# Optimization experiments

Measured on AMD Instinct MI355X. Metric: run time of the kernel, lower is better.

Reference implementation:

```python
import jax, jax.numpy as jnp
import numpy as np

IN_CH = 512
PROP_CH = 512
T_FEAT = 16384
T_FRAME = 32768
GROUPS = 32
EPS = 1e-5


def conv1x1(x, w, b):
    # x: (B, Cin, T), w: (Cout, Cin), b: (Cout,)
    return jnp.einsum('bct,oc->bot', x, w) + b[None, :, None]


def group_norm(x, gamma, beta):
    bsz, c, t = x.shape
    xg = x.reshape(bsz, GROUPS, c // GROUPS, t)
    mean = jnp.mean(xg, axis=(2, 3), keepdims=True)
    var = jnp.var(xg, axis=(2, 3), keepdims=True)
    xn = ((xg - mean) * jax.lax.rsqrt(var + EPS)).reshape(bsz, c, t)
    return xn * gamma[None, :, None] + beta[None, :, None]


def block(x, w, b, g, bt):
    # _Unit1D(k=1, act=None) -> GroupNorm(32) -> ReLU
    return jax.nn.relu(group_norm(conv1x1(x, w, b), g, bt))


def setup_inputs() -> dict:
    key = jax.random.key(0)
    ks = jax.random.split(key, 5)
    return dict(
        feature=jax.random.normal(ks[0], (1, IN_CH, T_FEAT), jnp.float32),
        frame_level_feature=jax.random.normal(ks[1], (1, IN_CH, T_FRAME), jnp.float32),
        cur_w=jax.random.normal(ks[2], (PROP_CH, IN_CH), jnp.float32) * 0.02,
        cur_b=jnp.zeros((PROP_CH,), jnp.float32),
        gn1_g=jnp.ones((PROP_CH,), jnp.float32),
        gn1_b=jnp.zeros((PROP_CH,), jnp.float32),
        lr_w=jax.random.normal(ks[3], (PROP_CH * 2, IN_CH), jnp.float32) * 0.02,
        lr_b=jnp.zeros((PROP_CH * 2,), jnp.float32),
        gn2_g=jnp.ones((PROP_CH * 2,), jnp.float32),
        gn2_b=jnp.zeros((PROP_CH * 2,), jnp.float32),
        prop_w=jax.random.normal(ks[4], (IN_CH, PROP_CH * 4), jnp.float32) * 0.02,
        prop_b=jnp.zeros((IN_CH,), jnp.float32),
        gn3_g=jnp.ones((IN_CH,), jnp.float32),
        gn3_b=jnp.zeros((IN_CH,), jnp.float32),
    )


def reference(feature, frame_level_feature, cur_w, cur_b, gn1_g, gn1_b,
              lr_w, lr_b, gn2_g, gn2_b, prop_w, prop_b, gn3_g, gn3_b):
    fm_short = block(feature, cur_w, cur_b, gn1_g, gn1_b)   # (1, P, t)
    feat = block(feature, lr_w, lr_b, gn2_g, gn2_b)         # (1, 2P, t)
    t = feat.shape[2]

    # ---- inverse-CDF sampling, vectorized equivalent of the original loop ----
    max_values = jnp.max(frame_level_feature, axis=1)        # (1, T)
    max_values = max_values / jnp.sum(max_values)
    cdf = jnp.cumsum(max_values, axis=1)[0]                  # (T,)
    c = (cdf * t).astype(jnp.int32)                          # trunc toward 0, like .int()
    # In the original, cur_idx advances only while no bin matches and is
    # never advanced after a successful match, so EVERY iteration i picks
    # the FIRST index whose bin equals the smallest value >= 0 present in c.
    big = jnp.iinfo(jnp.int32).max
    cur = jnp.min(jnp.where(c >= 0, c, big))
    idx = jnp.argmax(c == cur)                               # first occurrence
    col = jax.lax.dynamic_index_in_dim(frame_level_feature, idx, axis=2)  # (1, C, 1)
    sampled = jnp.broadcast_to(col, (col.shape[0], col.shape[1], t))      # (1, C, t)

    mixed = jnp.concatenate([sampled, feat, fm_short], axis=1)  # (1, 4P, t)
    mixed = block(mixed, prop_w, prop_b, gn3_g, gn3_b)          # (1, Cin, t)
    return mixed, feat
```

## Files before the change

### kernel.cpp

```cpp
#include <hip/hip_runtime.h>
#include <hip/hip_bf16.h>
#include <cstdint>
#include <cstddef>

#define TN   16384
#define TFR  32768
#define K1   512
#define M12  1536
#define M3   512

#define NSLOT 64

typedef __attribute__((ext_vector_type(8))) short short8;
typedef __attribute__((ext_vector_type(4))) float f32x4;

__device__ __forceinline__ unsigned short f2bf(float f) {
  __hip_bfloat16 h = __float2bfloat16(f);
  unsigned short u; __builtin_memcpy(&u, &h, 2); return u;
}
__device__ __forceinline__ float bf2f(unsigned short u) {
  __hip_bfloat16 h; __builtin_memcpy(&h, &u, 2); return __bfloat162float(h);
}

__global__ void prep_w(const float* __restrict__ cur_w, const float* __restrict__ cur_b,
                       const float* __restrict__ lr_w, const float* __restrict__ lr_b,
                       const float* __restrict__ prop_w,
                       unsigned short* __restrict__ w12, unsigned short* __restrict__ w3,
                       float* __restrict__ b12) {
  int i = blockIdx.x * blockDim.x + threadIdx.x;
  {
    int r = i >> 9, k = i & 511;
    float v = (r < 1024) ? lr_w[i] : cur_w[(r - 1024) * 512 + k];
    w12[i] = f2bf(v);
  }
  {
    int o = i / 1536, c = i - o * 1536;
    w3[i] = f2bf(prop_w[o * 2048 + 512 + c]);
  }
  if (i < M12) b12[i] = (i < 1024) ? lr_b[i] : cur_b[i - 1024];
}

__global__ void maxred(const float* __restrict__ fr, float* __restrict__ pm) {
  int b = blockIdx.x;
  int cchunk = b >> 7;
  int t = (b & 127) * 256 + threadIdx.x;
  int cs = cchunk * 64;
  float mx = -3.4e38f;
#pragma unroll 8
  for (int c = cs; c < cs + 64; ++c) mx = fmaxf(mx, fr[(size_t)c * TFR + t]);
  pm[(size_t)cchunk * TFR + t] = mx;
}

__global__ __launch_bounds__(1024) void scan_pick(const float* __restrict__ pm,
                                                  int* __restrict__ idxp) {
  __shared__ float sA[1024], sB[1024];
  __shared__ int si[1024];
  int tid = threadIdx.x;
  int base = tid * 32;
  float mv[32];
  float lsum = 0.f;
#pragma unroll
  for (int j = 0; j < 32; ++j) {
    int t = base + j;
    float mx = pm[t];
#pragma unroll
    for (int p = 1; p < 8; ++p) mx = fmaxf(mx, pm[(size_t)p * TFR + t]);
    mv[j] = mx; lsum += mx;
  }
  sA[tid] = lsum; __syncthreads();
  float* a = sA; float* b = sB;
  for (int d = 1; d < 1024; d <<= 1) {
    float v = a[tid];
    if (tid >= d) v += a[tid - d];
    b[tid] = v; __syncthreads();
    float* tmp = a; a = b; b = tmp;
  }
  float total = a[1023];
  float prev = (tid > 0) ? a[tid - 1] : 0.f;
  float inv = 1.0f / total;
  int cloc[32];
  int minc = 0x7fffffff;
  float run = prev;
#pragma unroll
  for (int j = 0; j < 32; ++j) {
    run += mv[j];
    int cj = (int)(run * inv * 16384.0f);
    cloc[j] = cj;
    if (cj >= 0 && cj < minc) minc = cj;
  }
  si[tid] = minc; __syncthreads();
  for (int d = 512; d >= 1; d >>= 1) { if (tid < d) si[tid] = min(si[tid], si[tid + d]); __syncthreads(); }
  int cur = si[0]; __syncthreads();
  int cand = 0x7fffffff;
#pragma unroll
  for (int j = 0; j < 32; ++j)
    if (cloc[j] == cur && cand == 0x7fffffff) cand = base + j;
  si[tid] = cand; __syncthreads();
  for (int d = 512; d >= 1; d >>= 1) { if (tid < d) si[tid] = min(si[tid], si[tid + d]); __syncthreads(); }
  if (tid == 0) idxp[0] = si[0];
}

__global__ void sample_const(const float* __restrict__ prop_w, const float* __restrict__ prop_b,
                             const float* __restrict__ frame, const int* __restrict__ idxp,
                             float* __restrict__ constb) {
  int o = blockIdx.x * blockDim.x + threadIdx.x;
  if (o >= 512) return;
  int idx = idxp[0];
  float acc = prop_b[o];
  for (int c = 0; c < 512; ++c)
    acc += prop_w[o * 2048 + c] * frame[(size_t)c * TFR + idx];
  constb[o] = acc;
}

__global__ __launch_bounds__(256) void transpose_feat(const float* __restrict__ X,
                                                      unsigned short* __restrict__ XT) {
  __shared__ float tile[64][65];
  int t0 = blockIdx.x * 64, c0 = blockIdx.y * 64;
  int tx = threadIdx.x & 63, ty = threadIdx.x >> 6;
#pragma unroll
  for (int r = 0; r < 16; ++r) {
    int c = c0 + ty * 16 + r;
    tile[ty * 16 + r][tx] = X[(size_t)c * TN + t0 + tx];
  }
  __syncthreads();
#pragma unroll
  for (int r = 0; r < 16; ++r) {
    int t = t0 + ty * 16 + r;
    XT[(size_t)t * K1 + c0 + tx] = f2bf(tile[tx][ty * 16 + r]);
  }
}

__global__ __launch_bounds__(256) void gemm_bf16(
    const unsigned short* __restrict__ XT,
    const unsigned short* __restrict__ Wb,
    const float* __restrict__ bias,
    unsigned short* __restrict__ Y,
    float* __restrict__ gsum, float* __restrict__ gss,
    int K, int M, int mode)
{
  __shared__ __attribute__((aligned(16))) unsigned short As[128 * 64];
  __shared__ __attribute__((aligned(16))) unsigned short Bs[128 * 64];
  const int tid = threadIdx.x;
  const int lane = tid & 63;
  const int w = tid >> 6;
  const int t0 = blockIdx.x * 128;
  const int c0 = blockIdx.y * 128;

  f32x4 acc[4][4] = {};
  const int lrow = lane & 15;
  const int lk = (lane >> 4) * 8;
  const int tb = (w >> 1) * 64, cb = (w & 1) * 64;

  const int Lbase = w * 4096 + lane * 16;
  const int srow0 = Lbase >> 7;
  const int scolb = (Lbase & 127) ^ ((srow0 & 7) << 4);

  for (int ks = 0; ks < K; ks += 64) {
    __syncthreads();
#pragma unroll
    for (int it = 0; it < 4; ++it) {
      int row = srow0 + it * 8;
      const char* ga = (const char*)(XT + (size_t)(t0 + row) * K + ks) + scolb;
      const char* gb = (const char*)(Wb + (size_t)(c0 + row) * K + ks) + scolb;
      char* la = (char*)As + w * 4096 + it * 1024;
      char* lb = (char*)Bs + w * 4096 + it * 1024;
      __builtin_amdgcn_global_load_lds(
          (const __attribute__((address_space(1))) unsigned int*)ga,
          (__attribute__((address_space(3))) unsigned int*)la, 16, 0, 0);
      __builtin_amdgcn_global_load_lds(
          (const __attribute__((address_space(1))) unsigned int*)gb,
          (__attribute__((address_space(3))) unsigned int*)lb, 16, 0, 0);
    }
    __syncthreads();
#pragma unroll
    for (int kk = 0; kk < 64; kk += 32) {
      short8 a[4], b[4];
#pragma unroll
      for (int i = 0; i < 4; ++i) {
        int r = tb + i * 16 + lrow;
        int cbyte = ((kk + lk) * 2) ^ ((r & 7) << 4);
        a[i] = *(const short8*)((const char*)As + r * 128 + cbyte);
      }
#pragma unroll
      for (int j = 0; j < 4; ++j) {
        int r = cb + j * 16 + lrow;
        int cbyte = ((kk + lk) * 2) ^ ((r & 7) << 4);
        b[j] = *(const short8*)((const char*)Bs + r * 128 + cbyte);
      }
#pragma unroll
      for (int i = 0; i < 4; ++i)
#pragma unroll
        for (int j = 0; j < 4; ++j)
          acc[i][j] = __builtin_amdgcn_mfma_f32_16x16x32_bf16(a[i], b[j], acc[i][j], 0, 0, 0);
    }
  }

  const int lq = (lane >> 4) * 4;
  const int slot = blockIdx.x & (NSLOT - 1);
#pragma unroll
  for (int j = 0; j < 4; ++j) {
    int c = c0 + cb + j * 16 + lrow;
    float bv = bias[c];
    float s = 0.f, ss = 0.f;
#pragma unroll
    for (int i = 0; i < 4; ++i) {
#pragma unroll
      for (int q = 0; q < 4; ++q) {
        float v = acc[i][j][q] + bv;
        s += v; ss += v * v;
        int t = t0 + tb + i * 16 + lq + q;
        Y[(size_t)t * M + c] = f2bf(v);
      }
    }
#pragma unroll
    for (int off = 32; off >= 1; off >>= 1) { s += __shfl_xor(s, off); ss += __shfl_xor(ss, off); }
    if (lane == 0) {
      int g = (mode == 0) ? ((c < 1024) ? (c >> 5) : (32 + ((c - 1024) >> 4))) : (c >> 4);
      atomicAdd(&gsum[g * NSLOT + slot], s);
      atomicAdd(&gss[g * NSLOT + slot], ss);
    }
  }
}

__global__ __launch_bounds__(256) void norm12(
    unsigned short* __restrict__ yz,
    const float* __restrict__ gsum, const float* __restrict__ gss,
    const float* __restrict__ gn1_g, const float* __restrict__ gn1_b,
    const float* __restrict__ gn2_g, const float* __restrict__ gn2_b,
    float* __restrict__ dfeat) {
  __shared__ float tile[64][65];
  int t0 = blockIdx.x * 64, c0 = blockIdx.y * 64;
  int tx = threadIdx.x & 63, ty = threadIdx.x >> 6;
  int c = c0 + tx;
  int g; float gm, gb, cnt;
  if (c < 1024) { g = c >> 5;               gm = gn2_g[c];        gb = gn2_b[c];        cnt = 524288.f; }
  else          { g = 32 + ((c - 1024) >> 4); gm = gn1_g[c - 1024]; gb = gn1_b[c - 1024]; cnt = 262144.f; }
  float s = 0.f, q = 0.f;
#pragma unroll
  for (int i = 0; i < NSLOT; ++i) { s += gsum[g * NSLOT + i]; q += gss[g * NSLOT + i]; }
  float mean = s / cnt;
  float var = q / cnt - mean * mean;
  float rstd = rsqrtf(var + 1e-5f);
#pragma unroll
  for (int r = 0; r < 16; ++r) {
    int t = t0 + ty * 16 + r;
    size_t off = (size_t)t * 1536 + c;
    float v = bf2f(yz[off]);
    v = (v - mean) * rstd * gm + gb;
    v = fmaxf(v, 0.f);
    yz[off] = f2bf(v);
    tile[tx][ty * 16 + r] = v;
  }
  if (c0 < 1024) {
    __syncthreads();
#pragma unroll
    for (int r = 0; r < 16; ++r) {
      int cc = c0 + ty * 16 + r;
      dfeat[(size_t)cc * TN + t0 + tx] = tile[ty * 16 + r][tx];
    }
  }
}

__global__ __launch_bounds__(256) void norm3(
    const unsigned short* __restrict__ y3,
    const float* __restrict__ gsum, const float* __restrict__ gss,
    const float* __restrict__ g3g, const float* __restrict__ g3b,
    float* __restrict__ dmix) {
  __shared__ float tile[64][65];
  int t0 = blockIdx.x * 64, c0 = blockIdx.y * 64;
  int tx = threadIdx.x & 63, ty = threadIdx.x >> 6;
  int c = c0 + tx;
  int g = c >> 4;
  float s = 0.f, q = 0.f;
#pragma unroll
  for (int i = 0; i < NSLOT; ++i) { s += gsum[g * NSLOT + i]; q += gss[g * NSLOT + i]; }
  float mean = s / 262144.f;
  float var = q / 262144.f - mean * mean;
  float rstd = rsqrtf(var + 1e-5f);
  float gm = g3g[c], gb = g3b[c];
#pragma unroll
  for (int r = 0; r < 16; ++r) {
    int t = t0 + ty * 16 + r;
    float v = bf2f(y3[(size_t)t * 512 + c]);
    v = (v - mean) * rstd * gm + gb;
    tile[tx][ty * 16 + r] = fmaxf(v, 0.f);
  }
  __syncthreads();
#pragma unroll
  for (int r = 0; r < 16; ++r) {
    int cc = c0 + ty * 16 + r;
    dmix[(size_t)cc * TN + t0 + tx] = tile[ty * 16 + r][tx];
  }
}

extern "C" void kernel_launch(void* const* d_in, const int* in_sizes, int n_in,
                              void* d_out, int out_size, void* d_ws, size_t ws_size,
                              hipStream_t stream) {
  const float* feature = (const float*)d_in[0];
  const float* frame   = (const float*)d_in[1];
  const float* cur_w   = (const float*)d_in[2];
  const float* cur_b   = (const float*)d_in[3];
  const float* gn1_g   = (const float*)d_in[4];
  const float* gn1_b   = (const float*)d_in[5];
  const float* lr_w    = (const float*)d_in[6];
  const float* lr_b    = (const float*)d_in[7];
  const float* gn2_g   = (const float*)d_in[8];
  const float* gn2_b   = (const float*)d_in[9];
  const float* prop_w  = (const float*)d_in[10];
  const float* prop_b  = (const float*)d_in[11];
  const float* gn3_g   = (const float*)d_in[12];
  const float* gn3_b   = (const float*)d_in[13];

  char* ws = (char*)d_ws;
  unsigned short* yzT   = (unsigned short*)(ws);
  unsigned short* featT = (unsigned short*)(ws + 50331648);
  unsigned short* y3T   = featT;
  unsigned short* w12   = (unsigned short*)(ws + 67108864);
  unsigned short* w3    = (unsigned short*)(ws + 68681728);
  float* b12    = (float*)(ws + 70254592);
  float* pm     = (float*)(ws + 70260736);
  float* s12    = (float*)(ws + 71309312);
  float* ss12   = s12 + 64 * NSLOT;
  float* s3     = (float*)(ws + 71342080);
  float* ss3    = s3 + 32 * NSLOT;
  float* constb = (float*)(ws + 71358464);
  int*   idxp   = (int*)(ws + 71360512);

  float* dmix  = (float*)d_out;
  float* dfeat = (float*)d_out + 8388608;

  hipMemsetAsync(ws + 71309312, 0, 49152, stream);

  hipLaunchKernelGGL(prep_w, dim3(3072), dim3(256), 0, stream,
                     cur_w, cur_b, lr_w, lr_b, prop_w, w12, w3, b12);
  hipLaunchKernelGGL(maxred, dim3(1024), dim3(256), 0, stream, frame, pm);
  hipLaunchKernelGGL(scan_pick, dim3(1), dim3(1024), 0, stream, pm, idxp);
  hipLaunchKernelGGL(transpose_feat, dim3(256, 8), dim3(256), 0, stream, feature, featT);
  hipLaunchKernelGGL(sample_const, dim3(2), dim3(256), 0, stream,
                     prop_w, prop_b, frame, idxp, constb);
  hipLaunchKernelGGL(gemm_bf16, dim3(128, 12), dim3(256), 0, stream,
                     featT, w12, b12, yzT, s12, ss12, 512, 1536, 0);
  hipLaunchKernelGGL(norm12, dim3(256, 24), dim3(256), 0, stream,
                     yzT, s12, ss12, gn1_g, gn1_b, gn2_g, gn2_b, dfeat);
  hipLaunchKernelGGL(gemm_bf16, dim3(128, 4), dim3(256), 0, stream,
                     yzT, w3, constb, y3T, s3, ss3, 1536, 512, 1);
  hipLaunchKernelGGL(norm3, dim3(256, 8), dim3(256), 0, stream,
                     y3T, s3, ss3, gn3_g, gn3_b, dmix);
}
```

Measured before the change: 425.9 us.

## Vectorize memory access in reductions, transpose, and norm kernels; precompute group stats

Several kernels switch to wide loads and stores: maxred reads float4, transpose_feat writes ushort4, and norm12/norm3 read short8 rows and write float4 columns through the shared tile. sample_const is reworked to stage the sampled column in shared memory and spread the dot products over 16 lanes per output across 32 blocks. New finalize kernels compute group mean and rstd once, so each norm block no longer re-sums 64 slots per thread. The aim is to cut memory transactions and redundant work, at the cost of two extra tiny launches and possible LDS bank conflicts in the new tile access patterns.

```diff
diff --git a/kernel.cpp b/kernel.cpp
--- a/kernel.cpp
+++ b/kernel.cpp
@@ -42,13 +42,17 @@
 
 __global__ void maxred(const float* __restrict__ fr, float* __restrict__ pm) {
   int b = blockIdx.x;
-  int cchunk = b >> 7;
-  int t = (b & 127) * 256 + threadIdx.x;
+  int cchunk = b >> 5;
+  int t = (b & 31) * 1024 + threadIdx.x * 4;
   int cs = cchunk * 64;
-  float mx = -3.4e38f;
+  float4 mx = make_float4(-3.4e38f, -3.4e38f, -3.4e38f, -3.4e38f);
 #pragma unroll 8
-  for (int c = cs; c < cs + 64; ++c) mx = fmaxf(mx, fr[(size_t)c * TFR + t]);
-  pm[(size_t)cchunk * TFR + t] = mx;
+  for (int c = cs; c < cs + 64; ++c) {
+    float4 v = *(const float4*)(fr + (size_t)c * TFR + t);
+    mx.x = fmaxf(mx.x, v.x); mx.y = fmaxf(mx.y, v.y);
+    mx.z = fmaxf(mx.z, v.z); mx.w = fmaxf(mx.w, v.w);
+  }
+  *(float4*)(pm + (size_t)cchunk * TFR + t) = mx;
 }
 
 __global__ __launch_bounds__(1024) void scan_pick(const float* __restrict__ pm,
@@ -100,16 +104,27 @@
   if (tid == 0) idxp[0] = si[0];
 }
 
-__global__ void sample_const(const float* __restrict__ prop_w, const float* __restrict__ prop_b,
-                             const float* __restrict__ frame, const int* __restrict__ idxp,
-                             float* __restrict__ constb) {
-  int o = blockIdx.x * blockDim.x + threadIdx.x;
-  if (o >= 512) return;
+__global__ __launch_bounds__(256) void sample_const(
+    const float* __restrict__ prop_w, const float* __restrict__ prop_b,
+    const float* __restrict__ frame, const int* __restrict__ idxp,
+    float* __restrict__ constb) {
+  __shared__ float sfr[512];
+  int tid = threadIdx.x;
   int idx = idxp[0];
-  float acc = prop_b[o];
-  for (int c = 0; c < 512; ++c)
-    acc += prop_w[o * 2048 + c] * frame[(size_t)c * TFR + idx];
-  constb[o] = acc;
+  for (int c = tid; c < 512; c += 256) sfr[c] = frame[(size_t)c * TFR + idx];
+  __syncthreads();
+  int o = blockIdx.x * 16 + (tid >> 4);
+  int cl = tid & 15;
+  float acc = 0.f;
+#pragma unroll
+  for (int i = 0; i < 8; ++i) {
+    int c = i * 64 + cl * 4;
+    float4 wv = *(const float4*)(prop_w + (size_t)o * 2048 + c);
+    acc += wv.x * sfr[c] + wv.y * sfr[c + 1] + wv.z * sfr[c + 2] + wv.w * sfr[c + 3];
+  }
+#pragma unroll
+  for (int off = 8; off >= 1; off >>= 1) acc += __shfl_xor(acc, off);
+  if (cl == 0) constb[o] = acc + prop_b[o];
 }
 
 __global__ __launch_bounds__(256) void transpose_feat(const float* __restrict__ X,
@@ -123,10 +138,17 @@
     tile[ty * 16 + r][tx] = X[(size_t)c * TN + t0 + tx];
   }
   __syncthreads();
-#pragma unroll
-  for (int r = 0; r < 16; ++r) {
-    int t = t0 + ty * 16 + r;
-    XT[(size_t)t * K1 + c0 + tx] = f2bf(tile[tx][ty * 16 + r]);
+  int c4 = (threadIdx.x & 15) * 4;
+  int tl0 = threadIdx.x >> 4;
+#pragma unroll
+  for (int p = 0; p < 4; ++p) {
+    int tl = tl0 + p * 16;
+    ushort4 o;
+    o.x = f2bf(tile[c4 + 0][tl]);
+    o.y = f2bf(tile[c4 + 1][tl]);
+    o.z = f2bf(tile[c4 + 2][tl]);
+    o.w = f2bf(tile[c4 + 3][tl]);
+    *(ushort4*)(XT + (size_t)(t0 + tl) * K1 + c0 + c4) = o;
   }
 }
 
@@ -222,74 +244,120 @@
   }
 }
 
+__global__ void finalize12(const float* __restrict__ gsum, const float* __restrict__ gss,
+                           float* __restrict__ mr) {
+  int g = threadIdx.x;
+  float s = 0.f, q = 0.f;
+#pragma unroll
+  for (int i = 0; i < NSLOT; ++i) { s += gsum[g * NSLOT + i]; q += gss[g * NSLOT + i]; }
+  float cnt = (g < 32) ? 524288.f : 262144.f;
+  float mean = s / cnt;
+  float var = q / cnt - mean * mean;
+  mr[g] = mean;
+  mr[64 + g] = rsqrtf(var + 1e-5f);
+}
+
+__global__ void finalize3(const float* __restrict__ gsum, const float* __restrict__ gss,
+                          float* __restrict__ mr) {
+  int g = threadIdx.x;
+  float s = 0.f, q = 0.f;
+#pragma unroll
+  for (int i = 0; i < NSLOT; ++i) { s += gsum[g * NSLOT + i]; q += gss[g * NSLOT + i]; }
+  float mean = s / 262144.f;
+  float var = q / 262144.f - mean * mean;
+  mr[g] = mean;
+  mr[32 + g] = rsqrtf(var + 1e-5f);
+}
+
 __global__ __launch_bounds__(256) void norm12(
     unsigned short* __restrict__ yz,
-    const float* __restrict__ gsum, const float* __restrict__ gss,
+    const float* __restrict__ mr,
     const float* __restrict__ gn1_g, const float* __restrict__ gn1_b,
     const float* __restrict__ gn2_g, const float* __restrict__ gn2_b,
     float* __restrict__ dfeat) {
   __shared__ float tile[64][65];
+  __shared__ float sgm[64], sgb[64], smean[64], srstd[64];
   int t0 = blockIdx.x * 64, c0 = blockIdx.y * 64;
-  int tx = threadIdx.x & 63, ty = threadIdx.x >> 6;
-  int c = c0 + tx;
-  int g; float gm, gb, cnt;
-  if (c < 1024) { g = c >> 5;               gm = gn2_g[c];        gb = gn2_b[c];        cnt = 524288.f; }
-  else          { g = 32 + ((c - 1024) >> 4); gm = gn1_g[c - 1024]; gb = gn1_b[c - 1024]; cnt = 262144.f; }
-  float s = 0.f, q = 0.f;
-#pragma unroll
-  for (int i = 0; i < NSLOT; ++i) { s += gsum[g * NSLOT + i]; q += gss[g * NSLOT + i]; }
-  float mean = s / cnt;
-  float var = q / cnt - mean * mean;
-  float rstd = rsqrtf(var + 1e-5f);
-#pragma unroll
-  for (int r = 0; r < 16; ++r) {
-    int t = t0 + ty * 16 + r;
-    size_t off = (size_t)t * 1536 + c;
-    float v = bf2f(yz[off]);
-    v = (v - mean) * rstd * gm + gb;
-    v = fmaxf(v, 0.f);
-    yz[off] = f2bf(v);
-    tile[tx][ty * 16 + r] = v;
+  int tid = threadIdx.x;
+  if (tid < 64) {
+    int c = c0 + tid;
+    int g; float gm, gb;
+    if (c < 1024) { g = c >> 5;                gm = gn2_g[c];        gb = gn2_b[c]; }
+    else          { g = 32 + ((c - 1024) >> 4); gm = gn1_g[c - 1024]; gb = gn1_b[c - 1024]; }
+    sgm[tid] = gm; sgb[tid] = gb; smean[tid] = mr[g]; srstd[tid] = mr[64 + g];
+  }
+  __syncthreads();
+  int c8 = (tid & 7) * 8;
+  int tl0 = tid >> 3;
+#pragma unroll
+  for (int p = 0; p < 2; ++p) {
+    int tl = tl0 + p * 32;
+    size_t off = (size_t)(t0 + tl) * 1536 + c0 + c8;
+    short8 v = *(const short8*)(yz + off);
+    short8 o;
+#pragma unroll
+    for (int e = 0; e < 8; ++e) {
+      int cl = c8 + e;
+      float f = bf2f((unsigned short)v[e]);
+      f = fmaxf((f - smean[cl]) * srstd[cl] * sgm[cl] + sgb[cl], 0.f);
+      o[e] = (short)f2bf(f);
+      tile[cl][tl] = f;
+    }
+    *(short8*)(yz + off) = o;
   }
   if (c0 < 1024) {
     __syncthreads();
-#pragma unroll
-    for (int r = 0; r < 16; ++r) {
-      int cc = c0 + ty * 16 + r;
-      dfeat[(size_t)cc * TN + t0 + tx] = tile[ty * 16 + r][tx];
+    int t4 = (tid & 15) * 4;
+    int cl0 = tid >> 4;
+#pragma unroll
+    for (int p = 0; p < 4; ++p) {
+      int cl = cl0 + p * 16;
+      float4 w;
+      w.x = tile[cl][t4 + 0]; w.y = tile[cl][t4 + 1];
+      w.z = tile[cl][t4 + 2]; w.w = tile[cl][t4 + 3];
+      *(float4*)(dfeat + (size_t)(c0 + cl) * TN + t0 + t4) = w;
     }
   }
 }
 
 __global__ __launch_bounds__(256) void norm3(
     const unsigned short* __restrict__ y3,
-    const float* __restrict__ gsum, const float* __restrict__ gss,
+    const float* __restrict__ mr,
     const float* __restrict__ g3g, const float* __restrict__ g3b,
     float* __restrict__ dmix) {
   __shared__ float tile[64][65];
+  __shared__ float sgm[64], sgb[64], smean[64], srstd[64];
   int t0 = blockIdx.x * 64, c0 = blockIdx.y * 64;
-  int tx = threadIdx.x & 63, ty = threadIdx.x >> 6;
-  int c = c0 + tx;
-  int g = c >> 4;
-  float s = 0.f, q = 0.f;
-#pragma unroll
-  for (int i = 0; i < NSLOT; ++i) { s += gsum[g * NSLOT + i]; q += gss[g * NSLOT + i]; }
-  float mean = s / 262144.f;
-  float var = q / 262144.f - mean * mean;
-  float rstd = rsqrtf(var + 1e-5f);
-  float gm = g3g[c], gb = g3b[c];
-#pragma unroll
-  for (int r = 0; r < 16; ++r) {
-    int t = t0 + ty * 16 + r;
-    float v = bf2f(y3[(size_t)t * 512 + c]);
-    v = (v - mean) * rstd * gm + gb;
-    tile[tx][ty * 16 + r] = fmaxf(v, 0.f);
+  int tid = threadIdx.x;
+  if (tid < 64) {
+    int c = c0 + tid;
+    int g = c >> 4;
+    sgm[tid] = g3g[c]; sgb[tid] = g3b[c]; smean[tid] = mr[g]; srstd[tid] = mr[32 + g];
   }
   __syncthreads();
-#pragma unroll
-  for (int r = 0; r < 16; ++r) {
-    int cc = c0 + ty * 16 + r;
-    dmix[(size_t)cc * TN + t0 + tx] = tile[ty * 16 + r][tx];
+  int c8 = (tid & 7) * 8;
+  int tl0 = tid >> 3;
+#pragma unroll
+  for (int p = 0; p < 2; ++p) {
+    int tl = tl0 + p * 32;
+    short8 v = *(const short8*)(y3 + (size_t)(t0 + tl) * 512 + c0 + c8);
+#pragma unroll
+    for (int e = 0; e < 8; ++e) {
+      int cl = c8 + e;
+      float f = bf2f((unsigned short)v[e]);
+      tile[cl][tl] = fmaxf((f - smean[cl]) * srstd[cl] * sgm[cl] + sgb[cl], 0.f);
+    }
+  }
+  __syncthreads();
+  int t4 = (tid & 15) * 4;
+  int cl0 = tid >> 4;
+#pragma unroll
+  for (int p = 0; p < 4; ++p) {
+    int cl = cl0 + p * 16;
+    float4 w;
+    w.x = tile[cl][t4 + 0]; w.y = tile[cl][t4 + 1];
+    w.z = tile[cl][t4 + 2]; w.w = tile[cl][t4 + 3];
+    *(float4*)(dmix + (size_t)(c0 + cl) * TN + t0 + t4) = w;
   }
 }
 
@@ -325,6 +393,8 @@
   float* ss3    = s3 + 32 * NSLOT;
   float* constb = (float*)(ws + 71358464);
   int*   idxp   = (int*)(ws + 71360512);
+  float* mr12   = (float*)(ws + 71360576);
+  float* mr3    = (float*)(ws + 71361088);
 
   float* dmix  = (float*)d_out;
   float* dfeat = (float*)d_out + 8388608;
@@ -333,17 +403,19 @@
 
   hipLaunchKernelGGL(prep_w, dim3(3072), dim3(256), 0, stream,
                      cur_w, cur_b, lr_w, lr_b, prop_w, w12, w3, b12);
-  hipLaunchKernelGGL(maxred, dim3(1024), dim3(256), 0, stream, frame, pm);
+  hipLaunchKernelGGL(maxred, dim3(256), dim3(256), 0, stream, frame, pm);
   hipLaunchKernelGGL(scan_pick, dim3(1), dim3(1024), 0, stream, pm, idxp);
   hipLaunchKernelGGL(transpose_feat, dim3(256, 8), dim3(256), 0, stream, feature, featT);
-  hipLaunchKernelGGL(sample_const, dim3(2), dim3(256), 0, stream,
+  hipLaunchKernelGGL(sample_const, dim3(32), dim3(256), 0, stream,
                      prop_w, prop_b, frame, idxp, constb);
   hipLaunchKernelGGL(gemm_bf16, dim3(128, 12), dim3(256), 0, stream,
                      featT, w12, b12, yzT, s12, ss12, 512, 1536, 0);
+  hipLaunchKernelGGL(finalize12, dim3(1), dim3(64), 0, stream, s12, ss12, mr12);
   hipLaunchKernelGGL(norm12, dim3(256, 24), dim3(256), 0, stream,
-                     yzT, s12, ss12, gn1_g, gn1_b, gn2_g, gn2_b, dfeat);
+                     yzT, mr12, gn1_g, gn1_b, gn2_g, gn2_b, dfeat);
   hipLaunchKernelGGL(gemm_bf16, dim3(128, 4), dim3(256), 0, stream,
                      yzT, w3, constb, y3T, s3, ss3, 1536, 512, 1);
+  hipLaunchKernelGGL(finalize3, dim3(1), dim3(32), 0, stream, s3, ss3, mr3);
   hipLaunchKernelGGL(norm3, dim3(256, 8), dim3(256), 0, stream,
-                     y3T, s3, ss3, gn3_g, gn3_b, dmix);
-}
+                     y3T, mr3, gn3_g, gn3_b, dmix);
+}
```

Result: faster. 380.6 us (-10.7%).
